# Performance work log

Measured on AMD Instinct MI355X. Metric: run time of the kernel, lower is better.

The kernel has to match this reference:

```python
import jax, jax.numpy as jnp
import numpy as np

D_MODEL = 1024
N_HEADS = 16


def get_freqs(seq, n_dim):
    # standard RoPE angles: (seq, n_dim//2)
    inv = 1.0 / (10000.0 ** (jnp.arange(0, n_dim, 2, dtype=jnp.float32) / n_dim))
    pos = jnp.arange(seq, dtype=jnp.float32)
    return pos[:, None] * inv[None, :]


def rope(x, freq):
    # x: (batch, seq, heads, n_dim); interleaved-pair rotation
    xf = x.astype(jnp.float32)
    x1 = xf[..., 0::2]
    x2 = xf[..., 1::2]
    cos = jnp.cos(freq)[None, :, None, :]  # (1, seq, 1, n_dim//2)
    sin = jnp.sin(freq)[None, :, None, :]
    r1 = x1 * cos - x2 * sin
    r2 = x1 * sin + x2 * cos
    out = jnp.stack([r1, r2], axis=-1).reshape(x.shape)
    return out.astype(x.dtype)


def setup_inputs() -> dict:
    key = jax.random.key(0)
    k1, k2, k3, k4, k5 = jax.random.split(key, 5)
    batch, seq = 2, 2048
    x = jax.random.normal(k1, (batch, seq, D_MODEL), dtype=jnp.float16)
    scale = jnp.float16(0.02)
    qw = jax.random.normal(k2, (D_MODEL, D_MODEL), dtype=jnp.float16) * scale
    kw = jax.random.normal(k3, (D_MODEL, D_MODEL), dtype=jnp.float16) * scale
    vw = jax.random.normal(k4, (D_MODEL, D_MODEL), dtype=jnp.float16) * scale
    ow = jax.random.normal(k5, (D_MODEL, D_MODEL), dtype=jnp.float16) * scale
    return {"x": x, "qw": qw, "kw": kw, "vw": vw, "ow": ow}


def reference(x, qw, kw, vw, ow):
    batch, seq, dim = x.shape
    n_heads = N_HEADS
    n_dim = dim // n_heads

    Q = (x @ qw).reshape(batch, seq, n_heads, n_dim)
    K = (x @ kw).reshape(batch, seq, n_heads, n_dim)
    V = (x @ vw).reshape(batch, seq, n_heads, n_dim)

    freq = get_freqs(seq, n_dim)
    Q = rope(Q, freq)
    K = rope(K, freq)

    Q = jnp.transpose(Q, (0, 2, 1, 3))  # (b, h, s, d)
    K = jnp.transpose(K, (0, 2, 1, 3))
    V = jnp.transpose(V, (0, 2, 1, 3))

    score = (Q @ jnp.swapaxes(K, -1, -2)) / jnp.sqrt(jnp.float16(dim))
    score = score.astype(jnp.float32)
    mask = jnp.tril(jnp.ones((1, 1, seq, seq), dtype=jnp.float32))
    score = score - 1e10 * (1.0 - mask)
    weights = jax.nn.softmax(score, axis=-1)  # fp32 (b, h, s, s)
    attn = weights @ V.astype(jnp.float32)

    merged = jnp.transpose(attn, (0, 2, 1, 3)).reshape(batch, seq, dim)
    out = merged @ ow.astype(jnp.float32)
    return out
```

## Files before the change

kernel.cpp:

```cpp
#include <hip/hip_runtime.h>
#include <math.h>

typedef _Float16 f16x8 __attribute__((ext_vector_type(8)));
typedef _Float16 f16x4 __attribute__((ext_vector_type(4)));
typedef float f32x4 __attribute__((ext_vector_type(4)));

#define SEQ 2048
#define DM 1024
#define NH 16
#define HD 64
#define MTOT 4096

#define NEG_BIG (-30000.0f)

__device__ __forceinline__ void gl_lds16(const _Float16* g, _Float16* l) {
  __builtin_amdgcn_global_load_lds(
      (const __attribute__((address_space(1))) unsigned int*)g,
      (__attribute__((address_space(3))) unsigned int*)l, 16, 0, 0);
}

__global__ __launch_bounds__(256) void convert_x(const float* __restrict__ src,
                                                 _Float16* __restrict__ dst) {
  const int i = (blockIdx.x * 256 + threadIdx.x) * 8;
  f32x4 a = *(const f32x4*)(src + i);
  f32x4 b = *(const f32x4*)(src + i + 4);
  f16x8 o;
#pragma unroll
  for (int j = 0; j < 4; ++j) { o[j] = (_Float16)a[j]; o[4 + j] = (_Float16)b[j]; }
  *(f16x8*)(dst + i) = o;
}

__global__ __launch_bounds__(256) void transpose_w(const float* __restrict__ q,
                                                   const float* __restrict__ k,
                                                   const float* __restrict__ v,
                                                   const float* __restrict__ o,
                                                   _Float16* __restrict__ dstBase) {
  __shared__ float Ts[64][65];
  const float* srcs[4] = {q, k, v, o};
  const float* src = srcs[blockIdx.z];
  _Float16* dst = dstBase + (size_t)blockIdx.z * DM * DM;
  const int t = threadIdx.x;
  const int k0 = blockIdx.y * 64, n0 = blockIdx.x * 64;
  const int r = t >> 2, c4 = (t & 3) * 16;
  const float* sp = src + (size_t)(k0 + r) * DM + n0 + c4;
#pragma unroll
  for (int j = 0; j < 4; ++j) {
    f32x4 vv = *(const f32x4*)(sp + j * 4);
#pragma unroll
    for (int e = 0; e < 4; ++e) Ts[r][c4 + j * 4 + e] = vv[e];
  }
  __syncthreads();
  f16x8 o0, o1;
#pragma unroll
  for (int j = 0; j < 8; ++j) {
    o0[j] = (_Float16)Ts[c4 + j][r];
    o1[j] = (_Float16)Ts[c4 + 8 + j][r];
  }
  _Float16* dp = dst + (size_t)(n0 + r) * DM + k0 + c4;
  *(f16x8*)(dp) = o0;
  *(f16x8*)(dp + 8) = o1;
}

template <bool FUSED3, bool OUTF32, bool ROPE>
__global__ __launch_bounds__(256) void gemm128(const _Float16* __restrict__ A,
                                               const _Float16* __restrict__ BT,
                                               void* __restrict__ Yv,
                                               int M, int K) {
  __shared__ _Float16 As[128 * 32];
  __shared__ _Float16 Bs[128 * 32];
  const int tid = threadIdx.x;
  const int lane = tid & 63;
  const int fl = lane & 15, fh = lane >> 4;
  const int wave = tid >> 6;
  const int m0 = blockIdx.y * 128;
  int n0 = blockIdx.x * 128;
  int mat = 0;
  const _Float16* Bp = BT;
  char* Yp = (char*)Yv;
  if (FUSED3) {
    mat = n0 >> 10;
    n0 &= 1023;
    Bp = BT + (size_t)mat * DM * DM;
    Yp += (size_t)mat * M * DM * (OUTF32 ? 4 : 2);
  }
  const int wm = (wave >> 1) * 64, wn = (wave & 1) * 64;

  const int l4 = lane >> 2, lc = (lane & 3) * 8;
  const _Float16* ga0 = A + (size_t)(m0 + wave * 32 + l4) * K + lc;
  const _Float16* ga1 = ga0 + (size_t)16 * K;
  const _Float16* gb0 = Bp + (size_t)(n0 + wave * 32 + l4) * K + lc;
  const _Float16* gb1 = gb0 + (size_t)16 * K;
  _Float16* la0 = &As[(wave * 32) * 32];
  _Float16* la1 = &As[(wave * 32 + 16) * 32];
  _Float16* lb0 = &Bs[(wave * 32) * 32];
  _Float16* lb1 = &Bs[(wave * 32 + 16) * 32];

  f32x4 acc[4][4] = {};

  for (int k0 = 0; k0 < K; k0 += 32) {
    __syncthreads();
    gl_lds16(ga0 + k0, la0);
    gl_lds16(ga1 + k0, la1);
    gl_lds16(gb0 + k0, lb0);
    gl_lds16(gb1 + k0, lb1);
    __syncthreads();
    f16x8 af[4], bf[4];
#pragma unroll
    for (int mi = 0; mi < 4; ++mi)
      af[mi] = *(const f16x8*)(&As[(wm + mi * 16 + fl) * 32 + fh * 8]);
#pragma unroll
    for (int ni = 0; ni < 4; ++ni)
      bf[ni] = *(const f16x8*)(&Bs[(wn + ni * 16 + fl) * 32 + fh * 8]);
#pragma unroll
    for (int mi = 0; mi < 4; ++mi)
#pragma unroll
      for (int ni = 0; ni < 4; ++ni)
        acc[mi][ni] = __builtin_amdgcn_mfma_f32_16x16x32_f16(af[mi], bf[ni], acc[mi][ni], 0, 0, 0);
  }

#pragma unroll
  for (int mi = 0; mi < 4; ++mi)
#pragma unroll
    for (int ni = 0; ni < 4; ++ni) {
      const int gm = m0 + wm + mi * 16 + fh * 4;
      const int gn = n0 + wn + ni * 16 + fl;
      if (ROPE && mat < 2) {
        const int d2 = (gn & 63) >> 1;
        const float inv = __powf(10000.0f, -(float)d2 * (1.0f / 32.0f));
        const float sgn = (gn & 1) ? 1.0f : -1.0f;
#pragma unroll
        for (int r = 0; r < 4; ++r) {
          const int s = (gm + r) & (SEQ - 1);
          float c, sn;
          __sincosf((float)s * inv, &sn, &c);
          const float v = acc[mi][ni][r];
          const float p = __shfl_xor(v, 1, 64);
          acc[mi][ni][r] = v * c + sgn * p * sn;
        }
      }
#pragma unroll
      for (int r = 0; r < 4; ++r) {
        if (OUTF32)
          ((float*)Yp)[(size_t)(gm + r) * DM + gn] = acc[mi][ni][r];
        else
          ((_Float16*)Yp)[(size_t)(gm + r) * DM + gn] = (_Float16)acc[mi][ni][r];
      }
    }
}

__device__ __forceinline__ void attn_tile(const _Float16 (*Ks)[72],
                                          const _Float16 (*Vt)[136],
                                          const f16x8 qf[2], f32x4 o_acc[4],
                                          float& m_r, float& l_r, int kv0,
                                          int qt, bool do_mask, int fl, int fh) {
  f32x4 s[8];
#pragma unroll
  for (int t = 0; t < 8; ++t) {
    f16x8 kf0 = *(const f16x8*)(&Ks[t * 16 + fl][fh * 8]);
    f16x8 kf1 = *(const f16x8*)(&Ks[t * 16 + fl][32 + fh * 8]);
    f32x4 z = {0.f, 0.f, 0.f, 0.f};
    z = __builtin_amdgcn_mfma_f32_16x16x32_f16(kf0, qf[0], z, 0, 0, 0);
    z = __builtin_amdgcn_mfma_f32_16x16x32_f16(kf1, qf[1], z, 0, 0, 0);
    s[t] = z;
  }
  const int qg = qt + fl;
  if (do_mask) {
#pragma unroll
    for (int t = 0; t < 8; ++t)
#pragma unroll
      for (int r = 0; r < 4; ++r)
        if (kv0 + t * 16 + fh * 4 + r > qg) s[t][r] = NEG_BIG;
  }
  float mx = s[0][0];
#pragma unroll
  for (int t = 0; t < 8; ++t)
#pragma unroll
    for (int r = 0; r < 4; ++r) mx = fmaxf(mx, s[t][r]);
  mx = fmaxf(mx, __shfl_xor(mx, 16, 64));
  mx = fmaxf(mx, __shfl_xor(mx, 32, 64));
  const float mn = fmaxf(m_r, mx);
  const float a = __expf(m_r - mn);
  float rs = 0.f;
  f16x4 pb[8];
#pragma unroll
  for (int t = 0; t < 8; ++t) {
    float p0 = __expf(s[t][0] - mn);
    float p1 = __expf(s[t][1] - mn);
    float p2 = __expf(s[t][2] - mn);
    float p3 = __expf(s[t][3] - mn);
    rs += (p0 + p1) + (p2 + p3);
    f16x4 pk = {(_Float16)p0, (_Float16)p1, (_Float16)p2, (_Float16)p3};
    pb[t] = pk;
  }
  rs += __shfl_xor(rs, 16, 64);
  rs += __shfl_xor(rs, 32, 64);
  l_r = l_r * a + rs;
  m_r = mn;
#pragma unroll
  for (int mt = 0; mt < 4; ++mt)
#pragma unroll
    for (int r = 0; r < 4; ++r) o_acc[mt][r] *= a;
#pragma unroll
  for (int mt = 0; mt < 4; ++mt)
#pragma unroll
    for (int t = 0; t < 8; ++t) {
      f16x4 va = *(const f16x4*)(&Vt[mt * 16 + fl][t * 16 + fh * 4]);
      o_acc[mt] = __builtin_amdgcn_mfma_f32_16x16x16f16(va, pb[t], o_acc[mt], 0, 0, 0);
    }
}

__global__ __launch_bounds__(512) void attn_kernel(const _Float16* __restrict__ Q,
                                                   const _Float16* __restrict__ K,
                                                   const _Float16* __restrict__ V,
                                                   _Float16* __restrict__ O) {
  __shared__ _Float16 Ks[128][72];
  __shared__ _Float16 Vt[64][136];

  const int tid = threadIdx.x;
  const int lane = tid & 63;
  const int fl = lane & 15, fh = lane >> 4;
  const int wave = tid >> 6;
  const int bh = blockIdx.y;
  const int b = bh >> 4, h = bh & 15;
  const int p = blockIdx.x;
  const int qt_lo = p * 128 + wave * 16;
  const int qt_hi = (15 - p) * 128 + wave * 16;

  const _Float16* Qb = Q + (size_t)b * SEQ * DM + h * HD;
  const _Float16* Kb = K + (size_t)b * SEQ * DM + h * HD;
  const _Float16* Vb = V + (size_t)b * SEQ * DM + h * HD;

  const _Float16 hs = (_Float16)0.03125f;
  f16x8 qlo[2], qhi[2];
#pragma unroll
  for (int kh = 0; kh < 2; ++kh) {
    qlo[kh] = *(const f16x8*)(Qb + (size_t)(qt_lo + fl) * DM + kh * 32 + fh * 8);
    qhi[kh] = *(const f16x8*)(Qb + (size_t)(qt_hi + fl) * DM + kh * 32 + fh * 8);
#pragma unroll
    for (int j = 0; j < 8; ++j) { qlo[kh][j] *= hs; qhi[kh][j] *= hs; }
  }

  f32x4 o_lo[4] = {}, o_hi[4] = {};
  float m_lo = NEG_BIG, l_lo = 0.f, m_hi = NEG_BIG, l_hi = 0.f;

  const int sr = tid >> 3, e = tid & 7, sc8 = e * 8;
  const int cmax = 15 - p;

  for (int c = 0; c <= cmax; ++c) {
    const int kv0 = c * 128;
    f16x8 k0v = *(const f16x8*)(Kb + (size_t)(kv0 + sr) * DM + sc8);
    f16x8 k1v = *(const f16x8*)(Kb + (size_t)(kv0 + 64 + sr) * DM + sc8);
    f16x8 v0v = *(const f16x8*)(Vb + (size_t)(kv0 + sr) * DM + sc8);
    f16x8 v1v = *(const f16x8*)(Vb + (size_t)(kv0 + 64 + sr) * DM + sc8);
    __syncthreads();
    *(f16x8*)(&Ks[sr][sc8]) = k0v;
    *(f16x8*)(&Ks[64 + sr][sc8]) = k1v;
#pragma unroll
    for (int t = 0; t < 8; ++t) {
      const int jj = (t + e) & 7;
      Vt[sc8 + jj][sr] = v0v[jj];
      Vt[sc8 + jj][64 + sr] = v1v[jj];
    }
    __syncthreads();

    attn_tile(Ks, Vt, qhi, o_hi, m_hi, l_hi, kv0, qt_hi, c == cmax, fl, fh);
    if (c <= p)
      attn_tile(Ks, Vt, qlo, o_lo, m_lo, l_lo, kv0, qt_lo, c == p, fl, fh);
  }

  {
    const float il = 1.0f / l_lo;
    _Float16* Op = O + ((size_t)b * SEQ + qt_lo + fl) * DM + h * HD;
#pragma unroll
    for (int mt = 0; mt < 4; ++mt) {
      f16x4 ov = {(_Float16)(o_lo[mt][0] * il), (_Float16)(o_lo[mt][1] * il),
                  (_Float16)(o_lo[mt][2] * il), (_Float16)(o_lo[mt][3] * il)};
      *(f16x4*)(Op + mt * 16 + fh * 4) = ov;
    }
  }
  {
    const float il = 1.0f / l_hi;
    _Float16* Op = O + ((size_t)b * SEQ + qt_hi + fl) * DM + h * HD;
#pragma unroll
    for (int mt = 0; mt < 4; ++mt) {
      f16x4 ov = {(_Float16)(o_hi[mt][0] * il), (_Float16)(o_hi[mt][1] * il),
                  (_Float16)(o_hi[mt][2] * il), (_Float16)(o_hi[mt][3] * il)};
      *(f16x4*)(Op + mt * 16 + fh * 4) = ov;
    }
  }
}

extern "C" void kernel_launch(void* const* d_in, const int* in_sizes, int n_in,
                              void* d_out, int out_size, void* d_ws, size_t ws_size,
                              hipStream_t stream) {
  const float* x = (const float*)d_in[0];
  const float* qw = (const float*)d_in[1];
  const float* kw = (const float*)d_in[2];
  const float* vw = (const float*)d_in[3];
  const float* ow = (const float*)d_in[4];
  float* out = (float*)d_out;

  const size_t MD = (size_t)MTOT * DM;
  _Float16* x16 = (_Float16*)d_ws;
  _Float16* wT = x16 + MD;
  _Float16* Qw = wT + 4 * (size_t)DM * DM;
  _Float16* Kw = Qw + MD;
  _Float16* Vw = Kw + MD;
  _Float16* Mw = x16;

  convert_x<<<MD / (256 * 8), 256, 0, stream>>>(x, x16);
  transpose_w<<<dim3(16, 16, 4), 256, 0, stream>>>(qw, kw, vw, ow, wT);

  gemm128<true, false, true><<<dim3(24, MTOT / 128), 256, 0, stream>>>(x16, wT, Qw, MTOT, DM);

  attn_kernel<<<dim3(8, 32), 512, 0, stream>>>(Qw, Kw, Vw, Mw);

  gemm128<false, true, false><<<dim3(8, MTOT / 128), 256, 0, stream>>>(
      Mw, wT + 3 * (size_t)DM * DM, out, MTOT, DM);
}
```

Baseline: 217.0 us.

## Merge prep kernels, deepen GEMM K-tile to 64, use smaller M tile for output projection

Folds the x conversion and the weight transpose into one prep launch, where extra z-slices handle the x conversion. The GEMM is templated on block size and now stages a K depth of 64 per iteration, which halves the number of barrier pairs and loads a full 128-byte row per 8 lanes. The output projection uses 64x128 tiles so it launches twice as many blocks. Costs are more LDS per block and a possible drop in occupancy.

```diff
diff --git a/kernel.cpp b/kernel.cpp
--- a/kernel.cpp
+++ b/kernel.cpp
@@ -19,27 +19,34 @@
       (__attribute__((address_space(3))) unsigned int*)l, 16, 0, 0);
 }
 
-__global__ __launch_bounds__(256) void convert_x(const float* __restrict__ src,
-                                                 _Float16* __restrict__ dst) {
-  const int i = (blockIdx.x * 256 + threadIdx.x) * 8;
-  f32x4 a = *(const f32x4*)(src + i);
-  f32x4 b = *(const f32x4*)(src + i + 4);
-  f16x8 o;
-#pragma unroll
-  for (int j = 0; j < 4; ++j) { o[j] = (_Float16)a[j]; o[4 + j] = (_Float16)b[j]; }
-  *(f16x8*)(dst + i) = o;
-}
-
-__global__ __launch_bounds__(256) void transpose_w(const float* __restrict__ q,
-                                                   const float* __restrict__ k,
-                                                   const float* __restrict__ v,
-                                                   const float* __restrict__ o,
-                                                   _Float16* __restrict__ dstBase) {
+__global__ __launch_bounds__(256) void prep(const float* __restrict__ x,
+                                            const float* __restrict__ qw,
+                                            const float* __restrict__ kw,
+                                            const float* __restrict__ vw,
+                                            const float* __restrict__ ow,
+                                            _Float16* __restrict__ x16,
+                                            _Float16* __restrict__ wT) {
+  const int z = blockIdx.z;
+  const int t = threadIdx.x;
+  if (z >= 4) {
+    const int c = (z - 4) * 256 + blockIdx.y * 16 + blockIdx.x;
+    const size_t base = (size_t)c * 8192;
+#pragma unroll
+    for (int rnd = 0; rnd < 4; ++rnd) {
+      const size_t i = base + rnd * 2048 + t * 8;
+      f32x4 a = *(const f32x4*)(x + i);
+      f32x4 b = *(const f32x4*)(x + i + 4);
+      f16x8 o;
+#pragma unroll
+      for (int j = 0; j < 4; ++j) { o[j] = (_Float16)a[j]; o[4 + j] = (_Float16)b[j]; }
+      *(f16x8*)(x16 + i) = o;
+    }
+    return;
+  }
   __shared__ float Ts[64][65];
-  const float* srcs[4] = {q, k, v, o};
-  const float* src = srcs[blockIdx.z];
-  _Float16* dst = dstBase + (size_t)blockIdx.z * DM * DM;
-  const int t = threadIdx.x;
+  const float* srcs[4] = {qw, kw, vw, ow};
+  const float* src = srcs[z];
+  _Float16* dst = wT + (size_t)z * DM * DM;
   const int k0 = blockIdx.y * 64, n0 = blockIdx.x * 64;
   const int r = t >> 2, c4 = (t & 3) * 16;
   const float* sp = src + (size_t)(k0 + r) * DM + n0 + c4;
@@ -61,19 +68,21 @@
   *(f16x8*)(dp + 8) = o1;
 }
 
-template <bool FUSED3, bool OUTF32, bool ROPE>
-__global__ __launch_bounds__(256) void gemm128(const _Float16* __restrict__ A,
-                                               const _Float16* __restrict__ BT,
-                                               void* __restrict__ Yv,
-                                               int M, int K) {
-  __shared__ _Float16 As[128 * 32];
-  __shared__ _Float16 Bs[128 * 32];
+template <int BM, int BN, bool FUSED3, bool OUTF32, bool ROPE>
+__global__ __launch_bounds__(256) void gemm_t(const _Float16* __restrict__ A,
+                                              const _Float16* __restrict__ BT,
+                                              void* __restrict__ Yv,
+                                              int M, int K) {
+  constexpr int WM = BM / 2, WN = BN / 2;
+  constexpr int MI = WM / 16, NI = WN / 16;
+  __shared__ _Float16 As[BM * 64];
+  __shared__ _Float16 Bs[BN * 64];
   const int tid = threadIdx.x;
   const int lane = tid & 63;
   const int fl = lane & 15, fh = lane >> 4;
   const int wave = tid >> 6;
-  const int m0 = blockIdx.y * 128;
-  int n0 = blockIdx.x * 128;
+  const int m0 = blockIdx.y * BM;
+  int n0 = blockIdx.x * BN;
   int mat = 0;
   const _Float16* Bp = BT;
   char* Yp = (char*)Yv;
@@ -83,45 +92,46 @@
     Bp = BT + (size_t)mat * DM * DM;
     Yp += (size_t)mat * M * DM * (OUTF32 ? 4 : 2);
   }
-  const int wm = (wave >> 1) * 64, wn = (wave & 1) * 64;
-
-  const int l4 = lane >> 2, lc = (lane & 3) * 8;
-  const _Float16* ga0 = A + (size_t)(m0 + wave * 32 + l4) * K + lc;
-  const _Float16* ga1 = ga0 + (size_t)16 * K;
-  const _Float16* gb0 = Bp + (size_t)(n0 + wave * 32 + l4) * K + lc;
-  const _Float16* gb1 = gb0 + (size_t)16 * K;
-  _Float16* la0 = &As[(wave * 32) * 32];
-  _Float16* la1 = &As[(wave * 32 + 16) * 32];
-  _Float16* lb0 = &Bs[(wave * 32) * 32];
-  _Float16* lb1 = &Bs[(wave * 32 + 16) * 32];
-
-  f32x4 acc[4][4] = {};
-
-  for (int k0 = 0; k0 < K; k0 += 32) {
+  const int wm = (wave >> 1) * WM, wn = (wave & 1) * WN;
+
+  const int srow = lane >> 3, scol = (lane & 7) * 8;
+
+  f32x4 acc[MI][NI] = {};
+
+  for (int k0 = 0; k0 < K; k0 += 64) {
     __syncthreads();
-    gl_lds16(ga0 + k0, la0);
-    gl_lds16(ga1 + k0, la1);
-    gl_lds16(gb0 + k0, lb0);
-    gl_lds16(gb1 + k0, lb1);
+#pragma unroll
+    for (int j = 0; j < BM / 32; ++j) {
+      const int rb = wave * 8 + j * 32;
+      gl_lds16(A + (size_t)(m0 + rb + srow) * K + k0 + scol, &As[rb * 64]);
+    }
+#pragma unroll
+    for (int j = 0; j < BN / 32; ++j) {
+      const int rb = wave * 8 + j * 32;
+      gl_lds16(Bp + (size_t)(n0 + rb + srow) * K + k0 + scol, &Bs[rb * 64]);
+    }
     __syncthreads();
-    f16x8 af[4], bf[4];
-#pragma unroll
-    for (int mi = 0; mi < 4; ++mi)
-      af[mi] = *(const f16x8*)(&As[(wm + mi * 16 + fl) * 32 + fh * 8]);
-#pragma unroll
-    for (int ni = 0; ni < 4; ++ni)
-      bf[ni] = *(const f16x8*)(&Bs[(wn + ni * 16 + fl) * 32 + fh * 8]);
-#pragma unroll
-    for (int mi = 0; mi < 4; ++mi)
-#pragma unroll
-      for (int ni = 0; ni < 4; ++ni)
-        acc[mi][ni] = __builtin_amdgcn_mfma_f32_16x16x32_f16(af[mi], bf[ni], acc[mi][ni], 0, 0, 0);
-  }
-
-#pragma unroll
-  for (int mi = 0; mi < 4; ++mi)
-#pragma unroll
-    for (int ni = 0; ni < 4; ++ni) {
+#pragma unroll
+    for (int kh = 0; kh < 2; ++kh) {
+      f16x8 af[MI], bf[NI];
+#pragma unroll
+      for (int mi = 0; mi < MI; ++mi)
+        af[mi] = *(const f16x8*)(&As[(wm + mi * 16 + fl) * 64 + kh * 32 + fh * 8]);
+#pragma unroll
+      for (int ni = 0; ni < NI; ++ni)
+        bf[ni] = *(const f16x8*)(&Bs[(wn + ni * 16 + fl) * 64 + kh * 32 + fh * 8]);
+#pragma unroll
+      for (int mi = 0; mi < MI; ++mi)
+#pragma unroll
+        for (int ni = 0; ni < NI; ++ni)
+          acc[mi][ni] = __builtin_amdgcn_mfma_f32_16x16x32_f16(af[mi], bf[ni], acc[mi][ni], 0, 0, 0);
+    }
+  }
+
+#pragma unroll
+  for (int mi = 0; mi < MI; ++mi)
+#pragma unroll
+    for (int ni = 0; ni < NI; ++ni) {
       const int gm = m0 + wm + mi * 16 + fh * 4;
       const int gn = n0 + wn + ni * 16 + fl;
       if (ROPE && mat < 2) {
@@ -308,13 +318,13 @@
   _Float16* Vw = Kw + MD;
   _Float16* Mw = x16;
 
-  convert_x<<<MD / (256 * 8), 256, 0, stream>>>(x, x16);
-  transpose_w<<<dim3(16, 16, 4), 256, 0, stream>>>(qw, kw, vw, ow, wT);
-
-  gemm128<true, false, true><<<dim3(24, MTOT / 128), 256, 0, stream>>>(x16, wT, Qw, MTOT, DM);
+  prep<<<dim3(16, 16, 6), 256, 0, stream>>>(x, qw, kw, vw, ow, x16, wT);
+
+  gemm_t<128, 128, true, false, true><<<dim3(24, MTOT / 128), 256, 0, stream>>>(
+      x16, wT, Qw, MTOT, DM);
 
   attn_kernel<<<dim3(8, 32), 512, 0, stream>>>(Qw, Kw, Vw, Mw);
 
-  gemm128<false, true, false><<<dim3(8, MTOT / 128), 256, 0, stream>>>(
+  gemm_t<64, 128, false, true, false><<<dim3(8, MTOT / 64), 256, 0, stream>>>(
       Mw, wT + 3 * (size_t)DM * DM, out, MTOT, DM);
 }
```

After: 215.5 us. Within noise of the previous version (-0.7%).
